# Kernel optimization log

Measured on AMD Instinct MI355X. Metric: run time of the kernel, lower is better.

The kernel has to match this reference:

```python
import jax, jax.numpy as jnp
import numpy as np

B, N, DIM = 2, 4096, 512
HEADS, HEAD_DIM = 8, 64
INNER = HEADS * HEAD_DIM


def setup_inputs() -> dict:
    key = jax.random.key(0)
    k1, k2, k3 = jax.random.split(key, 3)
    x = jax.random.normal(k1, (B, N, DIM), dtype=jnp.float32)
    w_qkv = jax.random.normal(k2, (DIM, 3 * INNER), dtype=jnp.float32) * (DIM ** -0.5)
    temperature = jnp.asarray(np.log(HEAD_DIM ** -0.5), dtype=jnp.float32)
    w_out = jax.random.normal(k3, (INNER, DIM), dtype=jnp.float32) * (INNER ** -0.5)
    b_out = jnp.zeros((DIM,), dtype=jnp.float32)
    return {"x": x, "w_qkv": w_qkv, "temperature": temperature, "w_out": w_out, "b_out": b_out}


def reference(x, w_qkv, temperature, w_out, b_out):
    b, n, _ = x.shape
    qkv = x @ w_qkv                                   # (B, N, 3*inner)
    q, k, v = jnp.split(qkv, 3, axis=-1)
    # Faithful to original: raw reshape (NOT transpose) into (B, H, N, d)
    q = q.reshape(b, HEADS, n, HEAD_DIM)
    k = k.reshape(b, HEADS, n, HEAD_DIM)
    v = v.reshape(b, HEADS, n, HEAD_DIM)
    scores = jnp.einsum('bhnd,bhmd->bhnm', q, k) * jnp.exp(temperature)
    mask = jnp.eye(n, dtype=bool)                     # diagonal self-mask
    mask_value = jnp.finfo(scores.dtype).min
    scores = jnp.where(mask, mask_value, scores)
    attn = jax.nn.softmax(scores, axis=-1)
    out = jnp.einsum('bhnm,bhmd->bhnd', attn, v)      # (B, H, N, d)
    # Faithful to original: raw reshape (NOT transpose) back to (B, N, H*d)
    out = out.reshape(b, n, HEADS * HEAD_DIM)
    return out @ w_out + b_out                        # dropout inactive at inference
```

## Files before the change

kernel.cpp:

```cpp
#include <hip/hip_runtime.h>


typedef __bf16 bf16;
typedef __bf16 bf16x8 __attribute__((ext_vector_type(8)));
typedef __bf16 bf16x4 __attribute__((ext_vector_type(4)));
typedef __bf16 bf16x2 __attribute__((ext_vector_type(2)));
typedef float  f32x4  __attribute__((ext_vector_type(4)));
typedef float  f32x16 __attribute__((ext_vector_type(16)));
typedef unsigned u32x4 __attribute__((ext_vector_type(4)));

#define MFMA_BF16(a, b, c)   __builtin_amdgcn_mfma_f32_16x16x32_bf16((a), (b), (c), 0, 0, 0)
#define MFMA32_BF16(a, b, c) __builtin_amdgcn_mfma_f32_32x32x16_bf16((a), (b), (c), 0, 0, 0)

__device__ __forceinline__ void gld_lds16(void* lds, const void* g) {
  __builtin_amdgcn_global_load_lds(
      (const __attribute__((address_space(1))) void*)g,
      (__attribute__((address_space(3))) void*)lds, 16, 0, 0);
}

__device__ __forceinline__ unsigned pkbf(float a, float b) {
  bf16x2 t; t[0] = (bf16)a; t[1] = (bf16)b;
  return __builtin_bit_cast(unsigned, t);
}


__global__ void cast4_kernel(const float* __restrict__ in, bf16* __restrict__ out, int n4) {
  int i = blockIdx.x * 256 + threadIdx.x;
  if (i >= n4) return;
  float4 v = ((const float4*)in)[i];
  bf16x4 o;
  o[0] = (bf16)v.x; o[1] = (bf16)v.y; o[2] = (bf16)v.z; o[3] = (bf16)v.w;
  *(bf16x4*)(out + 4 * i) = o;
}

__global__ void wtrans_kernel(const float* __restrict__ in, bf16* __restrict__ out, int C) {
  __shared__ float tile[64 * 65];
  const int t = threadIdx.x;
  const int c0 = blockIdx.x * 64, r0 = blockIdx.y * 64;
#pragma unroll
  for (int p = 0; p < 16; p++) {
    int idx = p * 256 + t, r = idx >> 6, c = idx & 63;
    tile[r * 65 + c] = in[(r0 + r) * C + c0 + c];
  }
  __syncthreads();
#pragma unroll
  for (int p = 0; p < 16; p++) {
    int idx = p * 256 + t, c = idx >> 6, r = idx & 63;
    out[(size_t)(c0 + c) * 512 + r0 + r] = (bf16)tile[r * 65 + c];
  }
}

__global__ void vtrans_kernel(const bf16* __restrict__ V, bf16* __restrict__ Vt) {
  __shared__ bf16 tile[64 * 65];
  const int t = threadIdx.x;
  const size_t base = (size_t)blockIdx.y << 18;
  const int n0 = blockIdx.x * 64;
#pragma unroll
  for (int p = 0; p < 16; p++) {
    int idx = p * 256 + t, r = idx >> 6, c = idx & 63;
    tile[r * 65 + c] = V[base + (size_t)(n0 + r) * 64 + c];
  }
  __syncthreads();
#pragma unroll
  for (int p = 0; p < 16; p++) {
    int idx = p * 256 + t, d = idx >> 6, n = idx & 63;
    Vt[base + (size_t)d * 4096 + n0 + n] = tile[n * 65 + d];
  }
}


template<int EPI, int WNT>
__global__ __launch_bounds__(256) void gemm_bt(
    const bf16* __restrict__ A, const bf16* __restrict__ Bt,
    bf16* __restrict__ oQ, bf16* __restrict__ oK, bf16* __restrict__ oV,
    float* __restrict__ oC, const float* __restrict__ bias,
    const float* __restrict__ temp)
{
  __shared__ bf16 As[128 * 32];
  __shared__ bf16 Bs[WNT * 32 * 32];

  const int t    = threadIdx.x;
  const int lane = t & 63;
  const int w    = t >> 6;
  const int mm   = lane & 15;
  const int q    = lane >> 4;
  const int wm   = w >> 1, wn = w & 1;
  const int m0   = blockIdx.y * 128;
  const int n0   = blockIdx.x * (WNT * 32);

  const int srow = t >> 2, sch = t & 3;
  const int gch  = sch ^ ((srow >> 1) & 3);
  const bf16* Ab = A  + (m0 + srow) * 512 + gch * 8;
  const bf16* Bb = Bt + (n0 + srow) * 512 + gch * 8;
  bf16* Asl = As + t * 8;
  bf16* Bsl = Bs + t * 8;

  const int fslot = (q ^ ((mm >> 1) & 3)) * 8;

  const f32x4 zero4 = {0.f, 0.f, 0.f, 0.f};
  f32x4 acc[4][WNT];
#pragma unroll
  for (int i = 0; i < 4; i++)
#pragma unroll
    for (int j = 0; j < WNT; j++) acc[i][j] = zero4;

  for (int k0 = 0; k0 < 512; k0 += 32) {
    __syncthreads();
    gld_lds16(Asl,        Ab + k0);
    gld_lds16(Asl + 2048, Ab + 64 * 512 + k0);
    gld_lds16(Bsl,        Bb + k0);
    if (WNT == 4) gld_lds16(Bsl + 2048, Bb + 64 * 512 + k0);
    __syncthreads();

    bf16x8 af[4], bfv[WNT];
#pragma unroll
    for (int i = 0; i < 4; i++)
      af[i] = *(const bf16x8*)(As + (wm * 64 + i * 16 + mm) * 32 + fslot);
#pragma unroll
    for (int j = 0; j < WNT; j++)
      bfv[j] = *(const bf16x8*)(Bs + (wn * (WNT * 16) + j * 16 + mm) * 32 + fslot);

#pragma unroll
    for (int i = 0; i < 4; i++)
#pragma unroll
      for (int j = 0; j < WNT; j++)
        acc[i][j] = MFMA_BF16(af[i], bfv[j], acc[i][j]);
  }

  if (EPI == 0) {
    const float scale = __expf(temp[0]) * 1.44269504088896f;
#pragma unroll
    for (int i = 0; i < 4; i++) {
      const int row = m0 + wm * 64 + i * 16 + q * 4;
#pragma unroll
      for (int j = 0; j < WNT; j++) {
        const int col = n0 + wn * (WNT * 16) + j * 16 + mm;
        bf16* dst; int c2; float s;
        if (col < 512)       { dst = oQ; c2 = col;        s = scale; }
        else if (col < 1024) { dst = oK; c2 = col - 512;  s = 1.0f;  }
        else                 { dst = oV; c2 = col - 1024; s = 1.0f;  }
#pragma unroll
        for (int r = 0; r < 4; r++)
          dst[(size_t)(row + r) * 512 + c2] = (bf16)(acc[i][j][r] * s);
      }
    }
  } else {
#pragma unroll
    for (int i = 0; i < 4; i++) {
      const int row = m0 + wm * 64 + i * 16 + q * 4;
#pragma unroll
      for (int j = 0; j < WNT; j++) {
        const int col = n0 + wn * (WNT * 16) + j * 16 + mm;
        const float b = bias[col];
#pragma unroll
        for (int r = 0; r < 4; r++)
          oC[(size_t)(row + r) * 512 + col] = acc[i][j][r] + b;
      }
    }
  }
}


template<int SPLIT>
__global__ __launch_bounds__(256, 4) void attn_kernel(
    const bf16* __restrict__ Q, const bf16* __restrict__ Kb,
    const bf16* __restrict__ Vt, bf16* __restrict__ O,
    float* __restrict__ Opart, float* __restrict__ Lpart)
{
  __shared__ bf16 Ks[2][64 * 64];
  __shared__ bf16 Vs[2][64 * 64];
  __shared__ float rsum[4][32];

  const int t    = threadIdx.x;
  const int lane = t & 63;
  const int w    = t >> 6;
  const int c32  = lane & 31;
  const int h    = lane >> 5;
  const int pxa  = (lane ^ 32) << 2;
  const int bh   = blockIdx.y;
  const int q0   = blockIdx.x * 128;
  const int z    = blockIdx.z;
  const size_t hb = (size_t)bh << 18;
  const bf16* Qh = Q  + hb;
  const bf16* Kh = Kb + hb;
  const bf16* Vh = Vt + hb;
  const int q0w  = q0 + w * 32;

  int tlo, tn;
  if (SPLIT == 1)      { tlo = 0;      tn = 64; }
  else                 { tlo = z * 32; tn = 32; }
  const int tmask = tn - 1;
  const int rot = (blockIdx.x * 5 + bh * 11 + z * 16) & tmask;

  bf16x8 qf[4];
#pragma unroll
  for (int s = 0; s < 4; s++)
    qf[s] = *(const bf16x8*)(Qh + (size_t)(q0w + c32) * 64 + s * 16 + h * 8);

  f32x16 o[2];
#pragma unroll
  for (int dt = 0; dt < 2; dt++)
#pragma unroll
    for (int r = 0; r < 16; r++) o[dt][r] = 0.f;
  float lacc = 0.f;

  const int r0 = t >> 3, c0 = t & 7;
  const int g0 = c0 ^ (r0 & 7);
  const bf16* Kg = Kh + (size_t)r0 * 64 + g0 * 8;
  const bf16* Vg = Vh + (size_t)r0 * 4096 + g0 * 8;

  const int dbase = q0w & ~63;
  const int kthalf = (q0w >> 5) & 1;

  {
    const int kv0 = (tlo + rot) * 64;
    gld_lds16(&Ks[0][t * 8],        Kg + (size_t)kv0 * 64);
    gld_lds16(&Ks[0][t * 8] + 2048, Kg + (size_t)(kv0 + 32) * 64);
    gld_lds16(&Vs[0][t * 8],        Vg + kv0);
    gld_lds16(&Vs[0][t * 8] + 2048, Vg + (size_t)32 * 4096 + kv0);
  }

  for (int it = 0; it < tn; it++) {
    const int cur = it & 1;
    {
      const int kvn = (tlo + ((it + 1 + rot) & tmask)) * 64;
      bf16* Kn = &Ks[cur ^ 1][t * 8];
      bf16* Vn = &Vs[cur ^ 1][t * 8];
      gld_lds16(Kn,        Kg + (size_t)kvn * 64);
      gld_lds16(Kn + 2048, Kg + (size_t)(kvn + 32) * 64);
      gld_lds16(Vn,        Vg + kvn);
      gld_lds16(Vn + 2048, Vg + (size_t)32 * 4096 + kvn);
    }
    __asm__ volatile("s_waitcnt vmcnt(4)" ::: "memory");
    __builtin_amdgcn_s_barrier();
    __asm__ volatile("" ::: "memory");

    const int kv0 = (tlo + ((it + rot) & tmask)) * 64;
    const bool diag = (kv0 == dbase);
    const bf16* Kc = Ks[cur];
    const bf16* Vc = Vs[cur];

    f32x16 sv0, sv1;
#pragma unroll
    for (int r = 0; r < 16; r++) { sv0[r] = 0.f; sv1[r] = 0.f; }
    {
      bf16x8 kf[4];
#pragma unroll
      for (int s = 0; s < 4; s++)
        kf[s] = *(const bf16x8*)(Kc + c32 * 64 + (((s << 1) | h) ^ (c32 & 7)) * 8);
#pragma unroll
      for (int s = 0; s < 4; s++)
        sv0 = MFMA32_BF16(kf[s], qf[s], sv0);
    }
    {
      const int kr = 32 + c32;
      bf16x8 kf[4];
#pragma unroll
      for (int s = 0; s < 4; s++)
        kf[s] = *(const bf16x8*)(Kc + kr * 64 + (((s << 1) | h) ^ (kr & 7)) * 8);
#pragma unroll
      for (int s = 0; s < 4; s++)
        sv1 = MFMA32_BF16(kf[s], qf[s], sv1);
    }

    if (diag) {
      if (kthalf == 0) {
#pragma unroll
        for (int r = 0; r < 16; r++)
          if (c32 == ((r & 3) + ((r >> 2) << 3) + (h << 2))) sv0[r] = -1e30f;
      } else {
#pragma unroll
        for (int r = 0; r < 16; r++)
          if (c32 == ((r & 3) + ((r >> 2) << 3) + (h << 2))) sv1[r] = -1e30f;
      }
    }

    bf16x8 pa00, pa01, pa10, pa11;
#pragma unroll
    for (int kt = 0; kt < 2; kt++) {
      float pp[16];
#pragma unroll
      for (int r = 0; r < 16; r++)
        pp[r] = __builtin_amdgcn_exp2f(kt ? sv1[r] : sv0[r]);
      float s8[8];
#pragma unroll
      for (int r = 0; r < 8; r++) s8[r] = pp[r] + pp[r + 8];
      float s4[4];
#pragma unroll
      for (int r = 0; r < 4; r++) s4[r] = s8[r] + s8[r + 4];
      lacc += (s4[0] + s4[1]) + (s4[2] + s4[3]);

#pragma unroll
      for (int s2 = 0; s2 < 2; s2++) {
        const int b = s2 * 8;
        unsigned wa = pkbf(pp[b + 0], pp[b + 1]);
        unsigned wc = pkbf(pp[b + 2], pp[b + 3]);
        unsigned wb = pkbf(pp[b + 4], pp[b + 5]);
        unsigned wd = pkbf(pp[b + 6], pp[b + 7]);
        unsigned r1 = (unsigned)__builtin_amdgcn_ds_bpermute(pxa, (int)(h ? wa : wb));
        unsigned r2 = (unsigned)__builtin_amdgcn_ds_bpermute(pxa, (int)(h ? wc : wd));
        u32x4 wv;
        wv[0] = h ? r1 : wa;
        wv[1] = h ? r2 : wc;
        wv[2] = h ? wb : r1;
        wv[3] = h ? wd : r2;
        bf16x8 pa = __builtin_bit_cast(bf16x8, wv);
        if (kt == 0) { if (s2 == 0) pa00 = pa; else pa01 = pa; }
        else         { if (s2 == 0) pa10 = pa; else pa11 = pa; }
      }
    }

#pragma unroll
    for (int kt = 0; kt < 2; kt++)
#pragma unroll
      for (int s2 = 0; s2 < 2; s2++) {
        const bf16x8 pa = kt ? (s2 ? pa11 : pa10) : (s2 ? pa01 : pa00);
        bf16x8 vf[2];
#pragma unroll
        for (int dt = 0; dt < 2; dt++) {
          const int d = dt * 32 + c32;
          vf[dt] = *(const bf16x8*)(Vc + d * 64 + (((((kt << 1) | s2) << 1) | h) ^ (d & 7)) * 8);
        }
#pragma unroll
        for (int dt = 0; dt < 2; dt++)
          o[dt] = MFMA32_BF16(pa, vf[dt], o[dt]);
      }

    __asm__ volatile("" ::: "memory");
    __builtin_amdgcn_s_barrier();
  }

  const int pb = __builtin_amdgcn_ds_bpermute(pxa, __builtin_bit_cast(int, lacc));
  const float tot = lacc + __builtin_bit_cast(float, pb);

  if (SPLIT == 1) {
    bf16* Oh = O + hb;
    if (h == 0) rsum[w][c32] = tot;
    __asm__ volatile("s_waitcnt lgkmcnt(0)" ::: "memory");
#pragma unroll
    for (int r = 0; r < 16; r++) {
      const int row = (r & 3) + ((r >> 2) << 3) + (h << 2);
      const float rinv = 1.0f / rsum[w][row];
#pragma unroll
      for (int dt = 0; dt < 2; dt++)
        Oh[(size_t)(q0w + row) * 64 + dt * 32 + c32] = (bf16)(o[dt][r] * rinv);
    }
  } else {
    float* Op = Opart + ((size_t)z << 22) + hb;
    float* Lp = Lpart + (z << 16) + (bh << 12);
    if (h == 0) Lp[q0w + c32] = tot;
#pragma unroll
    for (int r = 0; r < 16; r++) {
      const int row = (r & 3) + ((r >> 2) << 3) + (h << 2);
#pragma unroll
      for (int dt = 0; dt < 2; dt++)
        Op[(size_t)(q0w + row) * 64 + dt * 32 + c32] = o[dt][r];
    }
  }
}

template<int SPLIT>
__global__ void merge_kernel(const float* __restrict__ Op, const float* __restrict__ Lp,
                             bf16* __restrict__ Ob) {
  const int g = blockIdx.x * 256 + threadIdx.x;
  const int f = g * 4;
  const int row = f >> 6;
  float l = 0.f;
  float4 a = {0.f, 0.f, 0.f, 0.f};
#pragma unroll
  for (int zz = 0; zz < SPLIT; zz++) {
    l += Lp[(zz << 16) + row];
    const float4 b = *(const float4*)(Op + ((size_t)zz << 22) + f);
    a.x += b.x; a.y += b.y; a.z += b.z; a.w += b.w;
  }
  const float rinv = 1.0f / l;
  bf16x4 o;
  o[0] = (bf16)(a.x * rinv);
  o[1] = (bf16)(a.y * rinv);
  o[2] = (bf16)(a.z * rinv);
  o[3] = (bf16)(a.w * rinv);
  *(bf16x4*)(Ob + f) = o;
}


extern "C" void kernel_launch(void* const* d_in, const int* in_sizes, int n_in,
                              void* d_out, int out_size, void* d_ws, size_t ws_size,
                              hipStream_t stream) {
  const float* x      = (const float*)d_in[0];
  const float* w_qkv  = (const float*)d_in[1];
  const float* temp   = (const float*)d_in[2];
  const float* w_out  = (const float*)d_in[3];
  const float* b_out  = (const float*)d_in[4];
  float* out          = (float*)d_out;

  char* ws = (char*)d_ws;
  bf16*  Xb    = (bf16*)(ws);
  bf16*  Wt    = (bf16*)(ws + (size_t)(8u  << 20));
  bf16*  Qb    = (bf16*)(ws + (size_t)(10u << 20));
  bf16*  Kb    = (bf16*)(ws + (size_t)(18u << 20));
  bf16*  Vb    = (bf16*)(ws + (size_t)(26u << 20));
  bf16*  Vtb   = (bf16*)(ws + (size_t)(34u << 20));
  bf16*  Ob    = (bf16*)(ws + (size_t)(42u << 20));
  bf16*  Wot   = (bf16*)(ws + (size_t)(50u << 20));
  float* Lpart = (float*)(ws + (size_t)(51u << 20));
  float* Opart = (float*)(ws + (size_t)(52u << 20));

  const int split = (ws_size >= ((size_t)86u << 20)) ? 2 : 1;

  cast4_kernel<<<4096, 256, 0, stream>>>(x, Xb, (8192 * 512) / 4);
  wtrans_kernel<<<dim3(24, 8), 256, 0, stream>>>(w_qkv, Wt, 1536);
  wtrans_kernel<<<dim3(8, 8), 256, 0, stream>>>(w_out, Wot, 512);

  gemm_bt<0, 4><<<dim3(12, 64), 256, 0, stream>>>(Xb, Wt, Qb, Kb, Vb, nullptr, nullptr, temp);

  vtrans_kernel<<<dim3(64, 16), 256, 0, stream>>>(Vb, Vtb);

  if (split == 2) {
    attn_kernel<2><<<dim3(32, 16, 2), 256, 0, stream>>>(Qb, Kb, Vtb, nullptr, Opart, Lpart);
    merge_kernel<2><<<4096, 256, 0, stream>>>(Opart, Lpart, Ob);
  } else {
    attn_kernel<1><<<dim3(32, 16, 1), 256, 0, stream>>>(Qb, Kb, Vtb, Ob, nullptr, nullptr);
  }

  gemm_bt<1, 2><<<dim3(8, 64), 256, 0, stream>>>(Ob, Wot, nullptr, nullptr, nullptr, out, b_out, nullptr);
}
```

Baseline: 219.9 us.

## Software-pipeline PV MFMAs across iterations and drop split-KV merge path

Restructures the attention loop so that each iteration's P·V MFMAs are issued in the next iteration, overlapping them with the QK^T MFMAs and the softmax exp work. V fragments are read from LDS early into registers. The split-KV path and the merge kernel are removed, leaving a single 512-block launch with no KV rotation, and launch bounds drop to 2 blocks per SM to make room for the extra live registers. Trade-offs: higher register pressure, and lower parallelism than the previous split=2 launch when the workspace was large enough to select it.

```diff
diff --git a/kernel.cpp b/kernel.cpp
--- a/kernel.cpp
+++ b/kernel.cpp
@@ -161,11 +161,9 @@
 }
 
 
-template<int SPLIT>
-__global__ __launch_bounds__(256, 4) void attn_kernel(
+__global__ __launch_bounds__(256, 2) void attn_kernel(
     const bf16* __restrict__ Q, const bf16* __restrict__ Kb,
-    const bf16* __restrict__ Vt, bf16* __restrict__ O,
-    float* __restrict__ Opart, float* __restrict__ Lpart)
+    const bf16* __restrict__ Vt, bf16* __restrict__ O)
 {
   __shared__ bf16 Ks[2][64 * 64];
   __shared__ bf16 Vs[2][64 * 64];
@@ -179,19 +177,12 @@
   const int pxa  = (lane ^ 32) << 2;
   const int bh   = blockIdx.y;
   const int q0   = blockIdx.x * 128;
-  const int z    = blockIdx.z;
   const size_t hb = (size_t)bh << 18;
   const bf16* Qh = Q  + hb;
   const bf16* Kh = Kb + hb;
   const bf16* Vh = Vt + hb;
   const int q0w  = q0 + w * 32;
 
-  int tlo, tn;
-  if (SPLIT == 1)      { tlo = 0;      tn = 64; }
-  else                 { tlo = z * 32; tn = 32; }
-  const int tmask = tn - 1;
-  const int rot = (blockIdx.x * 5 + bh * 11 + z * 16) & tmask;
-
   bf16x8 qf[4];
 #pragma unroll
   for (int s = 0; s < 4; s++)
@@ -209,36 +200,48 @@
   const bf16* Kg = Kh + (size_t)r0 * 64 + g0 * 8;
   const bf16* Vg = Vh + (size_t)r0 * 4096 + g0 * 8;
 
-  const int dbase = q0w & ~63;
+  const int dtile  = q0w >> 6;
   const int kthalf = (q0w >> 5) & 1;
 
+  bf16x8 pap[2][2];
+  bf16x8 vfp[2][2][2];
+
   {
-    const int kv0 = (tlo + rot) * 64;
-    gld_lds16(&Ks[0][t * 8],        Kg + (size_t)kv0 * 64);
-    gld_lds16(&Ks[0][t * 8] + 2048, Kg + (size_t)(kv0 + 32) * 64);
-    gld_lds16(&Vs[0][t * 8],        Vg + kv0);
-    gld_lds16(&Vs[0][t * 8] + 2048, Vg + (size_t)32 * 4096 + kv0);
-  }
-
-  for (int it = 0; it < tn; it++) {
+    bf16* Kn = &Ks[0][t * 8];
+    bf16* Vn = &Vs[0][t * 8];
+    gld_lds16(Kn,        Kg);
+    gld_lds16(Kn + 2048, Kg + (size_t)32 * 64);
+    gld_lds16(Vn,        Vg);
+    gld_lds16(Vn + 2048, Vg + (size_t)32 * 4096);
+  }
+
+  for (int it = 0; it < 64; it++) {
     const int cur = it & 1;
     {
-      const int kvn = (tlo + ((it + 1 + rot) & tmask)) * 64;
+      const int kv = ((it + 1) & 63) * 64;
       bf16* Kn = &Ks[cur ^ 1][t * 8];
       bf16* Vn = &Vs[cur ^ 1][t * 8];
-      gld_lds16(Kn,        Kg + (size_t)kvn * 64);
-      gld_lds16(Kn + 2048, Kg + (size_t)(kvn + 32) * 64);
-      gld_lds16(Vn,        Vg + kvn);
-      gld_lds16(Vn + 2048, Vg + (size_t)32 * 4096 + kvn);
+      gld_lds16(Kn,        Kg + (size_t)kv * 64);
+      gld_lds16(Kn + 2048, Kg + (size_t)(kv + 32) * 64);
+      gld_lds16(Vn,        Vg + kv);
+      gld_lds16(Vn + 2048, Vg + (size_t)32 * 4096 + kv);
     }
     __asm__ volatile("s_waitcnt vmcnt(4)" ::: "memory");
     __builtin_amdgcn_s_barrier();
     __asm__ volatile("" ::: "memory");
 
-    const int kv0 = (tlo + ((it + rot) & tmask)) * 64;
-    const bool diag = (kv0 == dbase);
     const bf16* Kc = Ks[cur];
     const bf16* Vc = Vs[cur];
+
+    if (it) {
+#pragma unroll
+      for (int kt = 0; kt < 2; kt++)
+#pragma unroll
+        for (int s2 = 0; s2 < 2; s2++)
+#pragma unroll
+          for (int dt = 0; dt < 2; dt++)
+            o[dt] = MFMA32_BF16(pap[kt][s2], vfp[kt][s2][dt], o[dt]);
+    }
 
     f32x16 sv0, sv1;
 #pragma unroll
@@ -263,7 +266,18 @@
         sv1 = MFMA32_BF16(kf[s], qf[s], sv1);
     }
 
-    if (diag) {
+#pragma unroll
+    for (int kt = 0; kt < 2; kt++)
+#pragma unroll
+      for (int s2 = 0; s2 < 2; s2++)
+#pragma unroll
+        for (int dt = 0; dt < 2; dt++) {
+          const int d = dt * 32 + c32;
+          vfp[kt][s2][dt] =
+              *(const bf16x8*)(Vc + d * 64 + (((((kt << 1) | s2) << 1) | h) ^ (d & 7)) * 8);
+        }
+
+    if (it == dtile) {
       if (kthalf == 0) {
 #pragma unroll
         for (int r = 0; r < 16; r++)
@@ -275,7 +289,6 @@
       }
     }
 
-    bf16x8 pa00, pa01, pa10, pa11;
 #pragma unroll
     for (int kt = 0; kt < 2; kt++) {
       float pp[16];
@@ -304,82 +317,36 @@
         wv[1] = h ? r2 : wc;
         wv[2] = h ? wb : r1;
         wv[3] = h ? wd : r2;
-        bf16x8 pa = __builtin_bit_cast(bf16x8, wv);
-        if (kt == 0) { if (s2 == 0) pa00 = pa; else pa01 = pa; }
-        else         { if (s2 == 0) pa10 = pa; else pa11 = pa; }
+        pap[kt][s2] = __builtin_bit_cast(bf16x8, wv);
       }
     }
-
-#pragma unroll
-    for (int kt = 0; kt < 2; kt++)
-#pragma unroll
-      for (int s2 = 0; s2 < 2; s2++) {
-        const bf16x8 pa = kt ? (s2 ? pa11 : pa10) : (s2 ? pa01 : pa00);
-        bf16x8 vf[2];
-#pragma unroll
-        for (int dt = 0; dt < 2; dt++) {
-          const int d = dt * 32 + c32;
-          vf[dt] = *(const bf16x8*)(Vc + d * 64 + (((((kt << 1) | s2) << 1) | h) ^ (d & 7)) * 8);
-        }
-#pragma unroll
-        for (int dt = 0; dt < 2; dt++)
-          o[dt] = MFMA32_BF16(pa, vf[dt], o[dt]);
-      }
 
     __asm__ volatile("" ::: "memory");
     __builtin_amdgcn_s_barrier();
   }
 
+#pragma unroll
+  for (int kt = 0; kt < 2; kt++)
+#pragma unroll
+    for (int s2 = 0; s2 < 2; s2++)
+#pragma unroll
+      for (int dt = 0; dt < 2; dt++)
+        o[dt] = MFMA32_BF16(pap[kt][s2], vfp[kt][s2][dt], o[dt]);
+
   const int pb = __builtin_amdgcn_ds_bpermute(pxa, __builtin_bit_cast(int, lacc));
   const float tot = lacc + __builtin_bit_cast(float, pb);
 
-  if (SPLIT == 1) {
-    bf16* Oh = O + hb;
-    if (h == 0) rsum[w][c32] = tot;
-    __asm__ volatile("s_waitcnt lgkmcnt(0)" ::: "memory");
-#pragma unroll
-    for (int r = 0; r < 16; r++) {
-      const int row = (r & 3) + ((r >> 2) << 3) + (h << 2);
-      const float rinv = 1.0f / rsum[w][row];
-#pragma unroll
-      for (int dt = 0; dt < 2; dt++)
-        Oh[(size_t)(q0w + row) * 64 + dt * 32 + c32] = (bf16)(o[dt][r] * rinv);
-    }
-  } else {
-    float* Op = Opart + ((size_t)z << 22) + hb;
-    float* Lp = Lpart + (z << 16) + (bh << 12);
-    if (h == 0) Lp[q0w + c32] = tot;
-#pragma unroll
-    for (int r = 0; r < 16; r++) {
-      const int row = (r & 3) + ((r >> 2) << 3) + (h << 2);
-#pragma unroll
-      for (int dt = 0; dt < 2; dt++)
-        Op[(size_t)(q0w + row) * 64 + dt * 32 + c32] = o[dt][r];
-    }
-  }
-}
-
-template<int SPLIT>
-__global__ void merge_kernel(const float* __restrict__ Op, const float* __restrict__ Lp,
-                             bf16* __restrict__ Ob) {
-  const int g = blockIdx.x * 256 + threadIdx.x;
-  const int f = g * 4;
-  const int row = f >> 6;
-  float l = 0.f;
-  float4 a = {0.f, 0.f, 0.f, 0.f};
-#pragma unroll
-  for (int zz = 0; zz < SPLIT; zz++) {
-    l += Lp[(zz << 16) + row];
-    const float4 b = *(const float4*)(Op + ((size_t)zz << 22) + f);
-    a.x += b.x; a.y += b.y; a.z += b.z; a.w += b.w;
-  }
-  const float rinv = 1.0f / l;
-  bf16x4 o;
-  o[0] = (bf16)(a.x * rinv);
-  o[1] = (bf16)(a.y * rinv);
-  o[2] = (bf16)(a.z * rinv);
-  o[3] = (bf16)(a.w * rinv);
-  *(bf16x4*)(Ob + f) = o;
+  bf16* Oh = O + hb;
+  if (h == 0) rsum[w][c32] = tot;
+  __asm__ volatile("s_waitcnt lgkmcnt(0)" ::: "memory");
+#pragma unroll
+  for (int r = 0; r < 16; r++) {
+    const int row = (r & 3) + ((r >> 2) << 3) + (h << 2);
+    const float rinv = 1.0f / rsum[w][row];
+#pragma unroll
+    for (int dt = 0; dt < 2; dt++)
+      Oh[(size_t)(q0w + row) * 64 + dt * 32 + c32] = (bf16)(o[dt][r] * rinv);
+  }
 }
 
 
@@ -402,10 +369,6 @@
   bf16*  Vtb   = (bf16*)(ws + (size_t)(34u << 20));
   bf16*  Ob    = (bf16*)(ws + (size_t)(42u << 20));
   bf16*  Wot   = (bf16*)(ws + (size_t)(50u << 20));
-  float* Lpart = (float*)(ws + (size_t)(51u << 20));
-  float* Opart = (float*)(ws + (size_t)(52u << 20));
-
-  const int split = (ws_size >= ((size_t)86u << 20)) ? 2 : 1;
 
   cast4_kernel<<<4096, 256, 0, stream>>>(x, Xb, (8192 * 512) / 4);
   wtrans_kernel<<<dim3(24, 8), 256, 0, stream>>>(w_qkv, Wt, 1536);
@@ -415,12 +378,7 @@
 
   vtrans_kernel<<<dim3(64, 16), 256, 0, stream>>>(Vb, Vtb);
 
-  if (split == 2) {
-    attn_kernel<2><<<dim3(32, 16, 2), 256, 0, stream>>>(Qb, Kb, Vtb, nullptr, Opart, Lpart);
-    merge_kernel<2><<<4096, 256, 0, stream>>>(Opart, Lpart, Ob);
-  } else {
-    attn_kernel<1><<<dim3(32, 16, 1), 256, 0, stream>>>(Qb, Kb, Vtb, Ob, nullptr, nullptr);
-  }
+  attn_kernel<<<dim3(32, 16), 256, 0, stream>>>(Qb, Kb, Vtb, Ob);
 
   gemm_bt<1, 2><<<dim3(8, 64), 256, 0, stream>>>(Ob, Wot, nullptr, nullptr, nullptr, out, b_out, nullptr);
 }
```

New measurement: 205.4 us. -6.6%, faster.
